# Kernel optimization log

Hardware: AMD Instinct MI355X
Metric: run time of the kernel (lower is better)

Reference implementation:

```python
import jax, jax.numpy as jnp
from jax import lax
import numpy as np

IMG = 2048.0            # square image size (W=H)
STRIDES = [32, 64, 128]
FEATS = [64, 32, 16]    # IMG / stride
NUM_CLASSES = 80
BATCH = 8
SCORE_THRESH = 0.2
NMS_THRESH = 0.6
TOPK = 1000             # topk_candidates per level
DETS = 100              # detections_per_img


def make_anchors(fs, stride):
    # square anchors of size==stride centered on the feature grid (AnchorGenerator with ratio 1.0)
    c = (jnp.arange(fs, dtype=jnp.float32) + 0.5) * stride
    cy, cx = jnp.meshgrid(c, c, indexing='ij')
    cx, cy = cx.reshape(-1), cy.reshape(-1)
    h = stride / 2.0
    return jnp.stack([cx - h, cy - h, cx + h, cy + h], axis=1)


def setup_inputs() -> dict:
    key = jax.random.key(0)
    inp = {}
    for i, (fs, s) in enumerate(zip(FEATS, STRIDES)):
        hw = fs * fs
        key, k1, k2, k3 = jax.random.split(key, 4)
        inp[f'cls{i}'] = jax.random.normal(k1, (BATCH, hw, NUM_CLASSES), jnp.float32)
        inp[f'reg{i}'] = jax.random.uniform(k2, (BATCH, hw, 4), jnp.float32)
        inp[f'ctr{i}'] = jax.random.normal(k3, (BATCH, hw), jnp.float32)
        inp[f'anc{i}'] = make_anchors(fs, float(s))
    return inp


def _decode(rel, boxes):
    # BoxLinearCoder.decode_single with normalize_by_size=True
    cx = 0.5 * (boxes[:, 0] + boxes[:, 2])
    cy = 0.5 * (boxes[:, 1] + boxes[:, 3])
    w = boxes[:, 2] - boxes[:, 0]
    h = boxes[:, 3] - boxes[:, 1]
    rel = rel * jnp.stack([w, h, w, h], axis=1)
    return jnp.stack([cx - rel[:, 0], cy - rel[:, 1], cx + rel[:, 2], cy + rel[:, 3]], axis=1)


def _iou(b):
    # torchvision box_iou on a single set of boxes [N,4] -> [N,N]
    area = (b[:, 2] - b[:, 0]) * (b[:, 3] - b[:, 1])
    lt = jnp.maximum(b[:, None, :2], b[None, :, :2])
    rb = jnp.minimum(b[:, None, 2:], b[None, :, 2:])
    wh = jnp.clip(rb - lt, 0.0)
    inter = wh[..., 0] * wh[..., 1]
    return inter / (area[:, None] + area[None, :] - inter)


def _greedy_keep(iou):
    # classic greedy NMS on score-sorted boxes: suppress j>i with iou>thresh if i kept
    n = iou.shape[0]
    idx = jnp.arange(n)
    def body(i, keep):
        supp = keep[i] & (iou[i] > NMS_THRESH) & (idx > i)
        return keep & ~supp
    return lax.fori_loop(0, n, body, jnp.ones((n,), bool))


def _per_image(cls_l, reg_l, ctr_l, anc_l):
    boxes, scores, labels = [], [], []
    for cls, reg, ctr, anc in zip(cls_l, reg_l, ctr_l, anc_l):
        hw, c = cls.shape
        # scores = sqrt(sigmoid(cls) * sigmoid(ctrness)) flattened over anchors*classes
        sc = jnp.sqrt(jax.nn.sigmoid(cls) * jax.nn.sigmoid(ctr)[:, None]).reshape(-1)
        sc = jnp.where(sc > SCORE_THRESH, sc, -1.0)  # score threshold as mask (static shapes)
        ts, ti = lax.top_k(sc, TOPK)                 # per-level top-k candidates
        aidx = ti // c
        lab = ti % c
        b = jnp.clip(_decode(reg[aidx], anc[aidx]), 0.0, IMG)  # decode + clip to image
        boxes.append(b); scores.append(ts); labels.append(lab)
    boxes = jnp.concatenate(boxes)    # [3*TOPK, 4]
    scores = jnp.concatenate(scores)  # [3*TOPK]
    labels = jnp.concatenate(labels)  # [3*TOPK]
    n = scores.shape[0]
    # batched_nms via per-class coordinate offsets
    off = labels.astype(boxes.dtype) * (IMG + 1.0)
    ss, oi = lax.top_k(scores, n)     # sort candidates by score desc
    bs = boxes[oi] + off[oi][:, None]
    keep = lax.stop_gradient(_greedy_keep(_iou(bs)))
    fsc = jnp.where(keep & (ss > 0), ss, -1.0)
    fs, fi = lax.top_k(fsc, DETS)     # keep detections_per_img; score==-1 marks padding
    return boxes[oi][fi], fs, labels[oi][fi]


def reference(cls0, cls1, cls2, reg0, reg1, reg2, ctr0, ctr1, ctr2, anc0, anc1, anc2):
    f = jax.vmap(lambda c0, c1, c2, r0, r1, r2, t0, t1, t2: _per_image(
        [c0, c1, c2], [r0, r1, r2], [t0, t1, t2], [anc0, anc1, anc2]))
    return f(cls0, cls1, cls2, reg0, reg1, reg2, ctr0, ctr1, ctr2)
```

## Files before the change

### kernel.cpp

```cpp
#include <hip/hip_runtime.h>

#define NCLS  80
#define SELK  256
#define NLVL  3
#define NIMG  8
#define DETS  100
#define CAP   512
#define NDEC  512
#define NMSW  256
#define HBINS 4096
#define NHBLK 16
#define NCBLK 16
#define QBASE 0x3F800000u
#define QMAX  0x41C80000u
#define IMGSZ 2048.0f


__device__ __forceinline__ float sigm(float x) {
    if (x >= 0.f) return 1.f / (1.f + expf(-x));
    float e = expf(x);
    return e / (1.f + e);
}

__device__ __forceinline__ unsigned int qbits(float ea, float t1) {
    return __float_as_uint(__fmul_rn(__fadd_rn(1.f, ea), t1));
}

__device__ __forceinline__ unsigned long long shfl_u64(unsigned long long v, int lane) {
    int lo = (int)(unsigned int)v;
    int hi = (int)(unsigned int)(v >> 32);
    lo = __shfl(lo, lane, 64);
    hi = __shfl(hi, lane, 64);
    return ((unsigned long long)(unsigned int)hi << 32) | (unsigned int)lo;
}

__device__ __forceinline__ void lvl_select(int level,
    const float* c0, const float* c1, const float* c2,
    const float* t0, const float* t1, const float* t2,
    const float** cls, const float** ctr, int* hw) {
    if (level == 0)      { *cls = c0; *ctr = t0; *hw = 4096; }
    else if (level == 1) { *cls = c1; *ctr = t1; *hw = 1024; }
    else                 { *cls = c2; *ctr = t2; *hw = 256; }
}


__global__ void k_hist(const float* c0, const float* c1, const float* c2,
                       const float* t0, const float* t1, const float* t2,
                       unsigned int* parts, unsigned int* counters) {
    int level = blockIdx.z, img = blockIdx.y;
    int pair = img * NLVL + level;
    if (blockIdx.x == 0 && threadIdx.x == 0) counters[pair * 16] = 0;
    const float* cls; const float* ctr; int hw;
    lvl_select(level, c0, c1, c2, t0, t1, t2, &cls, &ctr, &hw);
    int n4 = hw * (NCLS / 4);
    const float4* cl4 = (const float4*)(cls + (size_t)img * hw * NCLS);
    const float* ct = ctr + (size_t)img * hw;
    __shared__ unsigned int h[HBINS];
    for (int i = threadIdx.x; i < HBINS; i += 256) h[i] = 0;
    __syncthreads();
    for (int i = blockIdx.x * 256 + threadIdx.x; i < n4; i += NHBLK * 256) {
        float4 v = cl4[i];
        int a = i / (NCLS / 4);
        float eb = expf(-ct[a]);
        float t1 = __fadd_rn(1.f, eb);
        #pragma unroll
        for (int k = 0; k < 4; ++k) {
            float x = (k == 0) ? v.x : (k == 1) ? v.y : (k == 2) ? v.z : v.w;
            unsigned int qb = qbits(expf(-x), t1);
            if (qb < QMAX) {
                unsigned int bin = (qb - QBASE) >> 13;
                if (bin > HBINS - 1) bin = HBINS - 1;
                atomicAdd(&h[bin], 1u);
            }
        }
    }
    __syncthreads();
    unsigned int* P = parts + ((size_t)(pair * NHBLK + blockIdx.x)) * HBINS;
    for (int i = threadIdx.x; i < HBINS; i += 256) P[i] = h[i];
}


__global__ void k_collect(const float* c0, const float* c1, const float* c2,
                          const float* t0, const float* t1, const float* t2,
                          const unsigned int* parts, unsigned int* counters,
                          unsigned long long* buf) {
    int level = blockIdx.z, img = blockIdx.y;
    int pair = img * NLVL + level;
    int tid = threadIdx.x;
    __shared__ unsigned int hb[HBINS];
    __shared__ unsigned int segsum[256];
    __shared__ unsigned int pref[256];
    __shared__ unsigned long long sbuf[CAP];
    __shared__ unsigned int scnt, sbase, Vsh;
    if (tid == 0) scnt = 0;
    {
        unsigned int acc[HBINS / 256];
        #pragma unroll
        for (int j = 0; j < HBINS / 256; ++j) acc[j] = 0;
        for (int blk = 0; blk < NHBLK; ++blk) {
            const unsigned int* P = parts + ((size_t)(pair * NHBLK + blk)) * HBINS;
            #pragma unroll
            for (int j = 0; j < HBINS / 256; ++j) acc[j] += P[tid + 256 * j];
        }
        #pragma unroll
        for (int j = 0; j < HBINS / 256; ++j) hb[tid + 256 * j] = acc[j];
    }
    __syncthreads();
    {
        unsigned int seg = 0;
        #pragma unroll
        for (int j = 0; j < 16; ++j) seg += hb[16 * tid + j];
        segsum[tid] = seg;
        pref[tid] = seg;
        __syncthreads();
        for (int off = 1; off < 256; off <<= 1) {
            unsigned int v = (tid >= off) ? pref[tid - off] : 0u;
            __syncthreads();
            pref[tid] += v;
            __syncthreads();
        }
        unsigned int incl = pref[tid];
        unsigned int excl = incl - segsum[tid];
        if (excl < (unsigned int)SELK && incl >= (unsigned int)SELK) {
            unsigned int cum = excl; int B = HBINS - 1;
            for (int b = 16 * tid; b < 16 * tid + 16; ++b) {
                cum += hb[b];
                if (cum >= (unsigned int)SELK) { B = b; break; }
            }
            Vsh = (B >= HBINS - 1) ? QMAX : (QBASE + ((unsigned int)(B + 1) << 13));
        }
        if (tid == 255 && pref[255] < (unsigned int)SELK)
            Vsh = QMAX;
    }
    __syncthreads();
    unsigned int V = Vsh;

    const float* cls; const float* ctr; int hw;
    lvl_select(level, c0, c1, c2, t0, t1, t2, &cls, &ctr, &hw);
    int n4 = hw * (NCLS / 4);
    const float4* cl4 = (const float4*)(cls + (size_t)img * hw * NCLS);
    const float* ct = ctr + (size_t)img * hw;
    for (int i = blockIdx.x * 256 + tid; i < n4; i += NCBLK * 256) {
        float4 v = cl4[i];
        int a = i / (NCLS / 4);
        float cta = ct[a];
        float eb = expf(-cta);
        float t1 = __fadd_rn(1.f, eb);
        #pragma unroll
        for (int k = 0; k < 4; ++k) {
            float x = (k == 0) ? v.x : (k == 1) ? v.y : (k == 2) ? v.z : v.w;
            unsigned int qb = qbits(expf(-x), t1);
            if (qb < V) {
                float s = sqrtf(sigm(x) * sigm(cta));
                unsigned int e = (unsigned int)(4 * i + k);
                unsigned int p = ((unsigned int)level << 19) | e;
                unsigned int slot = atomicAdd(&scnt, 1u);
                if (slot < CAP)
                    sbuf[slot] = ((unsigned long long)__float_as_uint(s) << 32) | (~p);
            }
        }
    }
    __syncthreads();
    unsigned int cl_n = scnt; if (cl_n > CAP) cl_n = CAP;
    if (tid == 0)
        sbase = atomicAdd(&counters[pair * 16], cl_n);
    __syncthreads();
    unsigned int base = sbase;
    for (unsigned int idx = tid; idx < cl_n; idx += 256) {
        unsigned int g = base + idx;
        if (g < CAP) buf[(size_t)pair * CAP + g] = sbuf[idx];
    }
}


__global__ void __launch_bounds__(512)
k_merge_nms(const unsigned long long* buf, const unsigned int* counters,
            const float* r0, const float* r1, const float* r2,
            const float* a0, const float* a1, const float* a2,
            float* out) {
    int img = blockIdx.x;
    int tid = threadIdx.x;
    int lane = tid & 63;
    __shared__ unsigned long long S[3 * CAP];
    __shared__ unsigned long long T[3 * CAP];
    __shared__ float4 wbox[NDEC];
    __shared__ int    wlab[NDEC];
    __shared__ float4 obx[NMSW];
    __shared__ float  oar[NMSW];
    __shared__ unsigned long long colmask[NMSW][4];
    __shared__ float4 sbx[64]; __shared__ float sar[64];
    __shared__ float4 koff[DETS]; __shared__ float karr[DETS];
    __shared__ float4 kb[DETS]; __shared__ float ks[DETS]; __shared__ int kl[DETS];
    __shared__ float4 rb[DETS]; __shared__ int rl[DETS];

    unsigned long long v0, v1, v2;
    {
        int c0n = (int)counters[(img * NLVL + 0) * 16]; if (c0n > CAP) c0n = CAP;
        int c1n = (int)counters[(img * NLVL + 1) * 16]; if (c1n > CAP) c1n = CAP;
        int c2n = (int)counters[(img * NLVL + 2) * 16]; if (c2n > CAP) c2n = CAP;
        v0 = (tid < c0n) ? buf[(size_t)(img * NLVL + 0) * CAP + tid] : 0ull;
        v1 = (tid < c1n) ? buf[(size_t)(img * NLVL + 1) * CAP + tid] : 0ull;
        v2 = (tid < c2n) ? buf[(size_t)(img * NLVL + 2) * CAP + tid] : 0ull;
    }
    #pragma unroll
    for (int k = 2; k <= 64; k <<= 1) {
        #pragma unroll
        for (int j = k >> 1; j > 0; j >>= 1) {
            unsigned long long p0 = shfl_u64(v0, lane ^ j);
            unsigned long long p1 = shfl_u64(v1, lane ^ j);
            unsigned long long p2 = shfl_u64(v2, lane ^ j);
            bool up = ((lane & k) == 0);
            bool lower = ((lane & j) == 0);
            bool mx = (up == lower);
            v0 = mx ? (v0 > p0 ? v0 : p0) : (v0 < p0 ? v0 : p0);
            v1 = mx ? (v1 > p1 ? v1 : p1) : (v1 < p1 ? v1 : p1);
            v2 = mx ? (v2 > p2 ? v2 : p2) : (v2 < p2 ? v2 : p2);
        }
    }
    S[0 * CAP + tid] = v0;
    S[1 * CAP + tid] = v1;
    S[2 * CAP + tid] = v2;
    __syncthreads();

    {
        unsigned long long* src = S;
        unsigned long long* dst = T;
        for (int m = 64; m <= 256; m <<= 1) {
            for (int o = tid; o < 3 * CAP; o += 512) {
                int seg = o >> 9, k = o & (CAP - 1);
                int pw = 2 * m;
                int ab = seg * CAP + (k / pw) * pw;
                int q = k % pw;
                int lo = max(0, q - m), hi = min(q, m);
                while (lo < hi) {
                    int mid = (lo + hi) >> 1;
                    if (src[ab + mid] > src[ab + m + (q - mid - 1)]) lo = mid + 1; else hi = mid;
                }
                int i2 = lo, j2 = q - lo;
                unsigned long long av = (i2 < m) ? src[ab + i2] : 0ull;
                unsigned long long bv = (j2 < m) ? src[ab + m + j2] : 0ull;
                dst[o] = (av > bv) ? av : bv;
            }
            __syncthreads();
            unsigned long long* tmp = src; src = dst; dst = tmp;
        }
    }
    for (int k = tid; k < 2 * CAP; k += 512) {
        int lo = max(0, k - CAP), hi = min(k, CAP);
        while (lo < hi) {
            int mid = (lo + hi) >> 1;
            if (T[mid] > T[CAP + (k - mid - 1)]) lo = mid + 1; else hi = mid;
        }
        int i = lo, j = k - lo;
        unsigned long long av = (i < CAP) ? T[i] : 0ull;
        unsigned long long bv = (j < CAP) ? T[CAP + j] : 0ull;
        S[k] = (av > bv) ? av : bv;
    }
    __syncthreads();
    {
        int k = tid;
        int lo = max(0, k - CAP), hi = k;
        while (lo < hi) {
            int mid = (lo + hi) >> 1;
            if (S[mid] > T[2 * CAP + (k - mid - 1)]) lo = mid + 1; else hi = mid;
        }
        int i = lo, j = k - lo;
        unsigned long long mv = (i < 2 * CAP) ? S[i] : 0ull;
        unsigned long long cv = (j < CAP) ? T[2 * CAP + j] : 0ull;
        unsigned long long rk = (mv > cv) ? mv : cv;
        __syncthreads();
        S[k] = rk;
    }
    __syncthreads();

    {
        unsigned long long key = S[tid];
        float4 b4 = make_float4(0.f, 0.f, 0.f, 0.f); int lbv = 0;
        if (key != 0ull) {
            unsigned int p = (~((unsigned int)key)) & 0x1FFFFFu;
            int lvl = (int)(p >> 19);
            unsigned int e = p & 0x7FFFFu;
            int a = (int)(e / NCLS); lbv = (int)(e % NCLS);
            const float* anc; const float* reg; int hw;
            if (lvl == 0)      { anc = a0; reg = r0; hw = 4096; }
            else if (lvl == 1) { anc = a1; reg = r1; hw = 1024; }
            else               { anc = a2; reg = r2; hw = 256; }
            const float* rg = reg + (size_t)img * hw * 4;
            float ax1 = anc[a * 4 + 0], ay1 = anc[a * 4 + 1];
            float ax2 = anc[a * 4 + 2], ay2 = anc[a * 4 + 3];
            float cx = 0.5f * (ax1 + ax2), cy = 0.5f * (ay1 + ay2);
            float w = ax2 - ax1, h = ay2 - ay1;
            float e0 = rg[a * 4 + 0] * w, e1 = rg[a * 4 + 1] * h;
            float e2 = rg[a * 4 + 2] * w, e3 = rg[a * 4 + 3] * h;
            b4.x = fminf(fmaxf(cx - e0, 0.f), IMGSZ);
            b4.y = fminf(fmaxf(cy - e1, 0.f), IMGSZ);
            b4.z = fminf(fmaxf(cx + e2, 0.f), IMGSZ);
            b4.w = fminf(fmaxf(cy + e3, 0.f), IMGSZ);
        }
        wbox[tid] = b4; wlab[tid] = lbv;
    }
    __syncthreads();

    if (tid < NMSW) {
        float4 bx = wbox[tid]; int lb = wlab[tid];
        float off = (float)lb * (IMGSZ + 1.0f);
        float ox1 = bx.x + off, oy1 = bx.y + off;
        float ox2 = bx.z + off, oy2 = bx.w + off;
        obx[tid] = make_float4(ox1, oy1, ox2, oy2);
        oar[tid] = (ox2 - ox1) * (oy2 - oy1);
    }
    __syncthreads();
    for (int Tk = tid; Tk < NMSW * 4; Tk += 512) {
        int j = Tk & (NMSW - 1);
        int w = Tk >> 8;
        float4 oj = obx[j]; float aj = oar[j];
        unsigned long long m = 0ull;
        int base = w * 64;
        for (int jj = 0; jj < 64; ++jj) {
            int i = base + jj;
            if (i < j) {
                float4 oi = obx[i]; float ai = oar[i];
                float lx = fmaxf(oi.x, oj.x), ly = fmaxf(oi.y, oj.y);
                float rx = fminf(oi.z, oj.z), ry = fminf(oi.w, oj.w);
                float ww = fmaxf(rx - lx, 0.f), hh = fmaxf(ry - ly, 0.f);
                float inter = ww * hh;
                if (inter / (ai + aj - inter) > 0.6f) m |= (1ull << jj);
            }
        }
        colmask[j][w] = m;
    }
    __syncthreads();

    if (tid >= 64) return;
    unsigned long long lmask_lt = (lane == 0) ? 0ull : (~0ull >> (64 - lane));
    unsigned long long K[4] = {0ull, 0ull, 0ull, 0ull};

    int kept = 0, ring = 0, r = 0;

    while (kept < DETS && r < NDEC) {
        int rank = r + lane;
        unsigned long long key = (rank < NDEC) ? S[rank] : 0ull;
        unsigned int bits = (unsigned int)(key >> 32);
        unsigned long long pm = __ballot(bits != 0u);
        int npos = (pm == ~0ull) ? 64 : (int)__builtin_ctzll(~pm);
        if (npos == 0) break;

        float4 bx = make_float4(0.f, 0.f, 0.f, 0.f); int lb = 0;
        if (lane < npos) { bx = wbox[rank]; lb = wlab[rank]; }
        float off = (float)lb * (IMGSZ + 1.0f);
        float ox1 = bx.x + off, oy1 = bx.y + off;
        float ox2 = bx.z + off, oy2 = bx.w + off;
        float car = (ox2 - ox1) * (oy2 - oy1);

        bool supk = false;
        unsigned long long col = 0ull;
        if (r < NMSW) {
            int b = r >> 6;
            int i = rank;
            unsigned long long cm0 = colmask[i][0], cm1 = colmask[i][1];
            unsigned long long cm2 = colmask[i][2], cm3 = colmask[i][3];
            unsigned long long sup = 0ull;
            if (b > 0) sup |= cm0 & K[0];
            if (b > 1) sup |= cm1 & K[1];
            if (b > 2) sup |= cm2 & K[2];
            supk = sup != 0ull;
            col = (b == 0) ? cm0 : (b == 1) ? cm1 : (b == 2) ? cm2 : cm3;
        } else {
            sbx[lane] = make_float4(ox1, oy1, ox2, oy2);
            sar[lane] = car;
            for (int k2 = 0; k2 < kept; ++k2) {
                float4 kk = koff[k2]; float ka = karr[k2];
                float lx = fmaxf(kk.x, ox1), ly = fmaxf(kk.y, oy1);
                float rx = fminf(kk.z, ox2), ry = fminf(kk.w, oy2);
                float w = fmaxf(rx - lx, 0.f), h = fmaxf(ry - ly, 0.f);
                float inter = w * h;
                supk = supk || (inter / (ka + car - inter) > 0.6f);
            }
            for (int i = 0; i < npos; ++i) {
                float4 c = sbx[i]; float ca = sar[i];
                float lx = fmaxf(c.x, ox1), ly = fmaxf(c.y, oy1);
                float rx = fminf(c.z, ox2), ry = fminf(c.w, oy2);
                float w = fmaxf(rx - lx, 0.f), h = fmaxf(ry - ly, 0.f);
                float inter = w * h;
                if ((inter / (ca + car - inter) > 0.6f) && (i < lane)) col |= (1ull << i);
            }
        }
        unsigned long long undecided = __ballot((lane < npos) && !supk);
        unsigned long long aliveSel = 0ull;
        int capleft = DETS - kept;
        int lastSlot = npos - 1;
        while (undecided) {
            int i = (int)__builtin_ctzll(undecided);
            aliveSel |= (1ull << i);
            undecided &= ~(1ull << i);
            if (--capleft == 0) { lastSlot = i; break; }
            unsigned long long row = __ballot(((col >> i) & 1ull) != 0ull);
            undecided &= ~row;
        }
        unsigned long long region = (lastSlot >= 63) ? ~0ull : ((1ull << (lastSlot + 1)) - 1ull);
        region &= (npos >= 64) ? ~0ull : ((1ull << npos) - 1ull);
        unsigned long long rejm = region & ~aliveSel;

        if (r < NMSW) K[r >> 6] = aliveSel;

        if ((aliveSel >> lane) & 1ull) {
            int ki = kept + (int)__popcll(aliveSel & lmask_lt);
            koff[ki] = make_float4(ox1, oy1, ox2, oy2); karr[ki] = car;
            kb[ki] = bx; ks[ki] = __uint_as_float(bits); kl[ki] = lb;
        }
        if ((rejm >> lane) & 1ull) {
            int ri = ring + (int)__popcll(rejm & lmask_lt);
            if (ri < DETS) { rb[ri] = bx; rl[ri] = lb; }
        }
        kept += (int)__popcll(aliveSel);
        ring += (int)__popcll(rejm);
        r += lastSlot + 1;
    }

    while (kept < DETS && ring < DETS && r < NDEC) {
        int rank = r + lane;
        if (rank < NDEC) {
            int ri = ring + lane;
            if (ri < DETS) { rb[ri] = wbox[rank]; rl[ri] = wlab[rank]; }
        }
        int take = NDEC - r; if (take > 64) take = 64;
        ring += take;
        r += 64;
    }

    for (int k = lane; k < DETS; k += 64) {
        float4 bxo; float scv; int lv;
        if (k < kept) { bxo = kb[k]; scv = ks[k]; lv = kl[k]; }
        else { int q = k - kept; bxo = rb[q]; scv = -1.0f; lv = rl[q]; }
        float* ob = out + ((size_t)img * DETS + k) * 4;
        ob[0] = bxo.x; ob[1] = bxo.y; ob[2] = bxo.z; ob[3] = bxo.w;
        out[NIMG * DETS * 4 + img * DETS + k] = scv;
        out[NIMG * DETS * 5 + img * DETS + k] = (float)lv;
    }
}


extern "C" void kernel_launch(void* const* d_in, const int* in_sizes, int n_in,
                              void* d_out, int out_size, void* d_ws, size_t ws_size,
                              hipStream_t stream) {
    (void)in_sizes; (void)n_in; (void)out_size; (void)ws_size;
    const float* cls0 = (const float*)d_in[0];
    const float* reg0 = (const float*)d_in[1];
    const float* ctr0 = (const float*)d_in[2];
    const float* anc0 = (const float*)d_in[3];
    const float* cls1 = (const float*)d_in[4];
    const float* reg1 = (const float*)d_in[5];
    const float* ctr1 = (const float*)d_in[6];
    const float* anc1 = (const float*)d_in[7];
    const float* cls2 = (const float*)d_in[8];
    const float* reg2 = (const float*)d_in[9];
    const float* ctr2 = (const float*)d_in[10];
    const float* anc2 = (const float*)d_in[11];
    float* out = (float*)d_out;
    char* ws = (char*)d_ws;

    const size_t OFF_PARTS = 0;
    const size_t OFF_CNT   = 6291456;
    const size_t OFF_BUF   = 6292992;

    unsigned int* parts = (unsigned int*)(ws + OFF_PARTS);
    unsigned int* cnt   = (unsigned int*)(ws + OFF_CNT);
    unsigned long long* buf = (unsigned long long*)(ws + OFF_BUF);

    k_hist<<<dim3(NHBLK, NIMG, NLVL), 256, 0, stream>>>(
        cls0, cls1, cls2, ctr0, ctr1, ctr2, parts, cnt);
    k_collect<<<dim3(NCBLK, NIMG, NLVL), 256, 0, stream>>>(
        cls0, cls1, cls2, ctr0, ctr1, ctr2, parts, cnt, buf);
    k_merge_nms<<<NIMG, 512, 0, stream>>>(buf, cnt, reg0, reg1, reg2,
                                          anc0, anc1, anc2, out);
}
```

Measured before the change: 163.1 us.

## Fuse histogram and collect into per-block local top-k with slab merge

Merges the histogram and collect kernels into one. Each block now finds its own local threshold from a private histogram and writes up to 48-64 candidates into a fixed per-block slab, which removes the global partial-histogram round trip, the atomic counters and one launch. The merge-NMS kernel now bitonic-sorts and merge-paths 1024 entries per level instead of 512, which adds work there. Picking candidates per block rather than per level could drop true top-k candidates if they cluster in one block's range, and the shared buffers are reused by aliasing to fit the larger pool.

```diff
diff --git a/kernel.cpp b/kernel.cpp
--- a/kernel.cpp
+++ b/kernel.cpp
@@ -1,16 +1,16 @@
 #include <hip/hip_runtime.h>
 
 #define NCLS  80
-#define SELK  256
+#define LLOC  48
+#define SCAP  64
 #define NLVL  3
 #define NIMG  8
 #define DETS  100
-#define CAP   512
+#define POOL  1024
 #define NDEC  512
 #define NMSW  256
 #define HBINS 4096
 #define NHBLK 16
-#define NCBLK 16
 #define QBASE 0x3F800000u
 #define QMAX  0x41C80000u
 #define IMGSZ 2048.0f
@@ -44,21 +44,26 @@
 }
 
 
-__global__ void k_hist(const float* c0, const float* c1, const float* c2,
-                       const float* t0, const float* t1, const float* t2,
-                       unsigned int* parts, unsigned int* counters) {
+__global__ void k_histcollect(const float* c0, const float* c1, const float* c2,
+                              const float* t0, const float* t1, const float* t2,
+                              unsigned long long* slab) {
     int level = blockIdx.z, img = blockIdx.y;
     int pair = img * NLVL + level;
-    if (blockIdx.x == 0 && threadIdx.x == 0) counters[pair * 16] = 0;
+    int tid = threadIdx.x;
     const float* cls; const float* ctr; int hw;
     lvl_select(level, c0, c1, c2, t0, t1, t2, &cls, &ctr, &hw);
     int n4 = hw * (NCLS / 4);
     const float4* cl4 = (const float4*)(cls + (size_t)img * hw * NCLS);
     const float* ct = ctr + (size_t)img * hw;
     __shared__ unsigned int h[HBINS];
-    for (int i = threadIdx.x; i < HBINS; i += 256) h[i] = 0;
-    __syncthreads();
-    for (int i = blockIdx.x * 256 + threadIdx.x; i < n4; i += NHBLK * 256) {
+    __shared__ unsigned int segsum[256];
+    __shared__ unsigned int pref[256];
+    __shared__ unsigned long long sbuf[SCAP];
+    __shared__ unsigned int scnt, Vsh;
+    if (tid == 0) scnt = 0;
+    for (int i = tid; i < HBINS; i += 256) h[i] = 0;
+    __syncthreads();
+    for (int i = blockIdx.x * 256 + tid; i < n4; i += NHBLK * 256) {
         float4 v = cl4[i];
         int a = i / (NCLS / 4);
         float eb = expf(-ct[a]);
@@ -75,41 +80,10 @@
         }
     }
     __syncthreads();
-    unsigned int* P = parts + ((size_t)(pair * NHBLK + blockIdx.x)) * HBINS;
-    for (int i = threadIdx.x; i < HBINS; i += 256) P[i] = h[i];
-}
-
-
-__global__ void k_collect(const float* c0, const float* c1, const float* c2,
-                          const float* t0, const float* t1, const float* t2,
-                          const unsigned int* parts, unsigned int* counters,
-                          unsigned long long* buf) {
-    int level = blockIdx.z, img = blockIdx.y;
-    int pair = img * NLVL + level;
-    int tid = threadIdx.x;
-    __shared__ unsigned int hb[HBINS];
-    __shared__ unsigned int segsum[256];
-    __shared__ unsigned int pref[256];
-    __shared__ unsigned long long sbuf[CAP];
-    __shared__ unsigned int scnt, sbase, Vsh;
-    if (tid == 0) scnt = 0;
-    {
-        unsigned int acc[HBINS / 256];
-        #pragma unroll
-        for (int j = 0; j < HBINS / 256; ++j) acc[j] = 0;
-        for (int blk = 0; blk < NHBLK; ++blk) {
-            const unsigned int* P = parts + ((size_t)(pair * NHBLK + blk)) * HBINS;
-            #pragma unroll
-            for (int j = 0; j < HBINS / 256; ++j) acc[j] += P[tid + 256 * j];
-        }
-        #pragma unroll
-        for (int j = 0; j < HBINS / 256; ++j) hb[tid + 256 * j] = acc[j];
-    }
-    __syncthreads();
     {
         unsigned int seg = 0;
         #pragma unroll
-        for (int j = 0; j < 16; ++j) seg += hb[16 * tid + j];
+        for (int j = 0; j < 16; ++j) seg += h[16 * tid + j];
         segsum[tid] = seg;
         pref[tid] = seg;
         __syncthreads();
@@ -121,26 +95,20 @@
         }
         unsigned int incl = pref[tid];
         unsigned int excl = incl - segsum[tid];
-        if (excl < (unsigned int)SELK && incl >= (unsigned int)SELK) {
+        if (excl < (unsigned int)LLOC && incl >= (unsigned int)LLOC) {
             unsigned int cum = excl; int B = HBINS - 1;
             for (int b = 16 * tid; b < 16 * tid + 16; ++b) {
-                cum += hb[b];
-                if (cum >= (unsigned int)SELK) { B = b; break; }
+                cum += h[b];
+                if (cum >= (unsigned int)LLOC) { B = b; break; }
             }
             Vsh = (B >= HBINS - 1) ? QMAX : (QBASE + ((unsigned int)(B + 1) << 13));
         }
-        if (tid == 255 && pref[255] < (unsigned int)SELK)
+        if (tid == 255 && pref[255] < (unsigned int)LLOC)
             Vsh = QMAX;
     }
     __syncthreads();
     unsigned int V = Vsh;
-
-    const float* cls; const float* ctr; int hw;
-    lvl_select(level, c0, c1, c2, t0, t1, t2, &cls, &ctr, &hw);
-    int n4 = hw * (NCLS / 4);
-    const float4* cl4 = (const float4*)(cls + (size_t)img * hw * NCLS);
-    const float* ct = ctr + (size_t)img * hw;
-    for (int i = blockIdx.x * 256 + tid; i < n4; i += NCBLK * 256) {
+    for (int i = blockIdx.x * 256 + tid; i < n4; i += NHBLK * 256) {
         float4 v = cl4[i];
         int a = i / (NCLS / 4);
         float cta = ct[a];
@@ -155,82 +123,86 @@
                 unsigned int e = (unsigned int)(4 * i + k);
                 unsigned int p = ((unsigned int)level << 19) | e;
                 unsigned int slot = atomicAdd(&scnt, 1u);
-                if (slot < CAP)
+                if (slot < SCAP)
                     sbuf[slot] = ((unsigned long long)__float_as_uint(s) << 32) | (~p);
             }
         }
     }
     __syncthreads();
-    unsigned int cl_n = scnt; if (cl_n > CAP) cl_n = CAP;
-    if (tid == 0)
-        sbase = atomicAdd(&counters[pair * 16], cl_n);
-    __syncthreads();
-    unsigned int base = sbase;
-    for (unsigned int idx = tid; idx < cl_n; idx += 256) {
-        unsigned int g = base + idx;
-        if (g < CAP) buf[(size_t)pair * CAP + g] = sbuf[idx];
-    }
+    unsigned int n = scnt; if (n > SCAP) n = SCAP;
+    unsigned long long* o = slab + ((size_t)(pair * NHBLK + blockIdx.x)) * SCAP;
+    for (unsigned int idx = tid; idx < SCAP; idx += 256)
+        o[idx] = (idx < n) ? sbuf[idx] : 0ull;
 }
 
 
 __global__ void __launch_bounds__(512)
-k_merge_nms(const unsigned long long* buf, const unsigned int* counters,
+k_merge_nms(const unsigned long long* slab,
             const float* r0, const float* r1, const float* r2,
             const float* a0, const float* a1, const float* a2,
             float* out) {
     int img = blockIdx.x;
     int tid = threadIdx.x;
     int lane = tid & 63;
-    __shared__ unsigned long long S[3 * CAP];
-    __shared__ unsigned long long T[3 * CAP];
-    __shared__ float4 wbox[NDEC];
-    __shared__ int    wlab[NDEC];
-    __shared__ float4 obx[NMSW];
-    __shared__ float  oar[NMSW];
-    __shared__ unsigned long long colmask[NMSW][4];
+    int w = tid >> 6;
+    __shared__ __align__(16) unsigned long long W0[3 * POOL];
+    __shared__ __align__(16) unsigned long long W1[3 * POOL];
     __shared__ float4 sbx[64]; __shared__ float sar[64];
     __shared__ float4 koff[DETS]; __shared__ float karr[DETS];
     __shared__ float4 kb[DETS]; __shared__ float ks[DETS]; __shared__ int kl[DETS];
     __shared__ float4 rb[DETS]; __shared__ int rl[DETS];
-
-    unsigned long long v0, v1, v2;
-    {
-        int c0n = (int)counters[(img * NLVL + 0) * 16]; if (c0n > CAP) c0n = CAP;
-        int c1n = (int)counters[(img * NLVL + 1) * 16]; if (c1n > CAP) c1n = CAP;
-        int c2n = (int)counters[(img * NLVL + 2) * 16]; if (c2n > CAP) c2n = CAP;
-        v0 = (tid < c0n) ? buf[(size_t)(img * NLVL + 0) * CAP + tid] : 0ull;
-        v1 = (tid < c1n) ? buf[(size_t)(img * NLVL + 1) * CAP + tid] : 0ull;
-        v2 = (tid < c2n) ? buf[(size_t)(img * NLVL + 2) * CAP + tid] : 0ull;
-    }
+    float4* wbox = (float4*)W0;
+    int*    wlab = (int*)((char*)W0 + 8192);
+    float4* obx  = (float4*)((char*)W0 + 10240);
+    float*  oar  = (float*)((char*)W0 + 14336);
+    unsigned long long (*colmask)[4] =
+        (unsigned long long (*)[4])((char*)W0 + 15360);
+
+    const unsigned long long* SL = slab + (size_t)img * NLVL * POOL;
+    unsigned long long v00 = SL[0 * POOL + (w    ) * 64 + lane];
+    unsigned long long v01 = SL[0 * POOL + (w + 8) * 64 + lane];
+    unsigned long long v10 = SL[1 * POOL + (w    ) * 64 + lane];
+    unsigned long long v11 = SL[1 * POOL + (w + 8) * 64 + lane];
+    unsigned long long v20 = SL[2 * POOL + (w    ) * 64 + lane];
+    unsigned long long v21 = SL[2 * POOL + (w + 8) * 64 + lane];
     #pragma unroll
     for (int k = 2; k <= 64; k <<= 1) {
         #pragma unroll
         for (int j = k >> 1; j > 0; j >>= 1) {
-            unsigned long long p0 = shfl_u64(v0, lane ^ j);
-            unsigned long long p1 = shfl_u64(v1, lane ^ j);
-            unsigned long long p2 = shfl_u64(v2, lane ^ j);
+            unsigned long long p00 = shfl_u64(v00, lane ^ j);
+            unsigned long long p01 = shfl_u64(v01, lane ^ j);
+            unsigned long long p10 = shfl_u64(v10, lane ^ j);
+            unsigned long long p11 = shfl_u64(v11, lane ^ j);
+            unsigned long long p20 = shfl_u64(v20, lane ^ j);
+            unsigned long long p21 = shfl_u64(v21, lane ^ j);
             bool up = ((lane & k) == 0);
             bool lower = ((lane & j) == 0);
             bool mx = (up == lower);
-            v0 = mx ? (v0 > p0 ? v0 : p0) : (v0 < p0 ? v0 : p0);
-            v1 = mx ? (v1 > p1 ? v1 : p1) : (v1 < p1 ? v1 : p1);
-            v2 = mx ? (v2 > p2 ? v2 : p2) : (v2 < p2 ? v2 : p2);
-        }
-    }
-    S[0 * CAP + tid] = v0;
-    S[1 * CAP + tid] = v1;
-    S[2 * CAP + tid] = v2;
-    __syncthreads();
+            v00 = mx ? (v00 > p00 ? v00 : p00) : (v00 < p00 ? v00 : p00);
+            v01 = mx ? (v01 > p01 ? v01 : p01) : (v01 < p01 ? v01 : p01);
+            v10 = mx ? (v10 > p10 ? v10 : p10) : (v10 < p10 ? v10 : p10);
+            v11 = mx ? (v11 > p11 ? v11 : p11) : (v11 < p11 ? v11 : p11);
+            v20 = mx ? (v20 > p20 ? v20 : p20) : (v20 < p20 ? v20 : p20);
+            v21 = mx ? (v21 > p21 ? v21 : p21) : (v21 < p21 ? v21 : p21);
+        }
+    }
+    W1[0 * POOL + (w    ) * 64 + lane] = v00;
+    W1[0 * POOL + (w + 8) * 64 + lane] = v01;
+    W1[1 * POOL + (w    ) * 64 + lane] = v10;
+    W1[1 * POOL + (w + 8) * 64 + lane] = v11;
+    W1[2 * POOL + (w    ) * 64 + lane] = v20;
+    W1[2 * POOL + (w + 8) * 64 + lane] = v21;
 
     {
-        unsigned long long* src = S;
-        unsigned long long* dst = T;
-        for (int m = 64; m <= 256; m <<= 1) {
-            for (int o = tid; o < 3 * CAP; o += 512) {
-                int seg = o >> 9, k = o & (CAP - 1);
+        unsigned long long* src = W1;
+        unsigned long long* dst = W0;
+        for (int m = 64; m <= 512; m <<= 1) {
+            __syncthreads();
+            for (int o = tid; o < 3 * POOL; o += 512) {
+                int seg = o >> 10, k = o & (POOL - 1);
                 int pw = 2 * m;
-                int ab = seg * CAP + (k / pw) * pw;
-                int q = k % pw;
+                int ab = seg * POOL + (k & ~(pw - 1));
+                int q = k & (pw - 1);
                 int lo = max(0, q - m), hi = min(q, m);
                 while (lo < hi) {
                     int mid = (lo + hi) >> 1;
@@ -241,40 +213,43 @@
                 unsigned long long bv = (j2 < m) ? src[ab + m + j2] : 0ull;
                 dst[o] = (av > bv) ? av : bv;
             }
-            __syncthreads();
             unsigned long long* tmp = src; src = dst; dst = tmp;
         }
     }
-    for (int k = tid; k < 2 * CAP; k += 512) {
-        int lo = max(0, k - CAP), hi = min(k, CAP);
+    __syncthreads();
+    {
+        int k = tid;
+        int lo = 0, hi = k;
         while (lo < hi) {
             int mid = (lo + hi) >> 1;
-            if (T[mid] > T[CAP + (k - mid - 1)]) lo = mid + 1; else hi = mid;
+            if (W1[mid] > W1[POOL + (k - mid - 1)]) lo = mid + 1; else hi = mid;
         }
         int i = lo, j = k - lo;
-        unsigned long long av = (i < CAP) ? T[i] : 0ull;
-        unsigned long long bv = (j < CAP) ? T[CAP + j] : 0ull;
-        S[k] = (av > bv) ? av : bv;
+        unsigned long long av = W1[i];
+        unsigned long long bv = W1[POOL + j];
+        unsigned long long rk = (av > bv) ? av : bv;
+        __syncthreads();
+        W1[k] = rk;
     }
     __syncthreads();
     {
         int k = tid;
-        int lo = max(0, k - CAP), hi = k;
+        int lo = 0, hi = k;
         while (lo < hi) {
             int mid = (lo + hi) >> 1;
-            if (S[mid] > T[2 * CAP + (k - mid - 1)]) lo = mid + 1; else hi = mid;
+            if (W1[mid] > W1[2 * POOL + (k - mid - 1)]) lo = mid + 1; else hi = mid;
         }
         int i = lo, j = k - lo;
-        unsigned long long mv = (i < 2 * CAP) ? S[i] : 0ull;
-        unsigned long long cv = (j < CAP) ? T[2 * CAP + j] : 0ull;
-        unsigned long long rk = (mv > cv) ? mv : cv;
+        unsigned long long av = (i < 512) ? W1[i] : 0ull;
+        unsigned long long bv = W1[2 * POOL + j];
+        unsigned long long rk = (av > bv) ? av : bv;
         __syncthreads();
-        S[k] = rk;
+        W1[POOL + k] = rk;
     }
     __syncthreads();
 
     {
-        unsigned long long key = S[tid];
+        unsigned long long key = W1[POOL + tid];
         float4 b4 = make_float4(0.f, 0.f, 0.f, 0.f); int lbv = 0;
         if (key != 0ull) {
             unsigned int p = (~((unsigned int)key)) & 0x1FFFFFu;
@@ -289,9 +264,9 @@
             float ax1 = anc[a * 4 + 0], ay1 = anc[a * 4 + 1];
             float ax2 = anc[a * 4 + 2], ay2 = anc[a * 4 + 3];
             float cx = 0.5f * (ax1 + ax2), cy = 0.5f * (ay1 + ay2);
-            float w = ax2 - ax1, h = ay2 - ay1;
-            float e0 = rg[a * 4 + 0] * w, e1 = rg[a * 4 + 1] * h;
-            float e2 = rg[a * 4 + 2] * w, e3 = rg[a * 4 + 3] * h;
+            float w2 = ax2 - ax1, h2 = ay2 - ay1;
+            float e0 = rg[a * 4 + 0] * w2, e1 = rg[a * 4 + 1] * h2;
+            float e2 = rg[a * 4 + 2] * w2, e3 = rg[a * 4 + 3] * h2;
             b4.x = fminf(fmaxf(cx - e0, 0.f), IMGSZ);
             b4.y = fminf(fmaxf(cy - e1, 0.f), IMGSZ);
             b4.z = fminf(fmaxf(cx + e2, 0.f), IMGSZ);
@@ -312,10 +287,10 @@
     __syncthreads();
     for (int Tk = tid; Tk < NMSW * 4; Tk += 512) {
         int j = Tk & (NMSW - 1);
-        int w = Tk >> 8;
+        int wq = Tk >> 8;
         float4 oj = obx[j]; float aj = oar[j];
         unsigned long long m = 0ull;
-        int base = w * 64;
+        int base = wq * 64;
         for (int jj = 0; jj < 64; ++jj) {
             int i = base + jj;
             if (i < j) {
@@ -327,7 +302,7 @@
                 if (inter / (ai + aj - inter) > 0.6f) m |= (1ull << jj);
             }
         }
-        colmask[j][w] = m;
+        colmask[j][wq] = m;
     }
     __syncthreads();
 
@@ -339,7 +314,7 @@
 
     while (kept < DETS && r < NDEC) {
         int rank = r + lane;
-        unsigned long long key = (rank < NDEC) ? S[rank] : 0ull;
+        unsigned long long key = (rank < NDEC) ? W1[POOL + rank] : 0ull;
         unsigned int bits = (unsigned int)(key >> 32);
         unsigned long long pm = __ballot(bits != 0u);
         int npos = (pm == ~0ull) ? 64 : (int)__builtin_ctzll(~pm);
@@ -372,16 +347,16 @@
                 float4 kk = koff[k2]; float ka = karr[k2];
                 float lx = fmaxf(kk.x, ox1), ly = fmaxf(kk.y, oy1);
                 float rx = fminf(kk.z, ox2), ry = fminf(kk.w, oy2);
-                float w = fmaxf(rx - lx, 0.f), h = fmaxf(ry - ly, 0.f);
-                float inter = w * h;
+                float w2 = fmaxf(rx - lx, 0.f), h2 = fmaxf(ry - ly, 0.f);
+                float inter = w2 * h2;
                 supk = supk || (inter / (ka + car - inter) > 0.6f);
             }
             for (int i = 0; i < npos; ++i) {
                 float4 c = sbx[i]; float ca = sar[i];
                 float lx = fmaxf(c.x, ox1), ly = fmaxf(c.y, oy1);
                 float rx = fminf(c.z, ox2), ry = fminf(c.w, oy2);
-                float w = fmaxf(rx - lx, 0.f), h = fmaxf(ry - ly, 0.f);
-                float inter = w * h;
+                float w2 = fmaxf(rx - lx, 0.f), h2 = fmaxf(ry - ly, 0.f);
+                float inter = w2 * h2;
                 if ((inter / (ca + car - inter) > 0.6f) && (i < lane)) col |= (1ull << i);
             }
         }
@@ -459,18 +434,10 @@
     float* out = (float*)d_out;
     char* ws = (char*)d_ws;
 
-    const size_t OFF_PARTS = 0;
-    const size_t OFF_CNT   = 6291456;
-    const size_t OFF_BUF   = 6292992;
-
-    unsigned int* parts = (unsigned int*)(ws + OFF_PARTS);
-    unsigned int* cnt   = (unsigned int*)(ws + OFF_CNT);
-    unsigned long long* buf = (unsigned long long*)(ws + OFF_BUF);
-
-    k_hist<<<dim3(NHBLK, NIMG, NLVL), 256, 0, stream>>>(
-        cls0, cls1, cls2, ctr0, ctr1, ctr2, parts, cnt);
-    k_collect<<<dim3(NCBLK, NIMG, NLVL), 256, 0, stream>>>(
-        cls0, cls1, cls2, ctr0, ctr1, ctr2, parts, cnt, buf);
-    k_merge_nms<<<NIMG, 512, 0, stream>>>(buf, cnt, reg0, reg1, reg2,
+    unsigned long long* slab = (unsigned long long*)ws;
+
+    k_histcollect<<<dim3(NHBLK, NIMG, NLVL), 256, 0, stream>>>(
+        cls0, cls1, cls2, ctr0, ctr1, ctr2, slab);
+    k_merge_nms<<<NIMG, 512, 0, stream>>>(slab, reg0, reg1, reg2,
                                           anc0, anc1, anc2, out);
 }
```

After: 162.5 us. Within noise of the previous version (-0.4%).
